# Performance work log

Hardware: AMD Instinct MI355X
Metric: run time of the kernel (lower is better)

## Reference

```python
import jax, jax.numpy as jnp
import numpy as np

B, H, W, C = 64, 56, 56, 256
ROUTES = 4
CONV_OUT = 64


def setup_inputs() -> dict:
    key = jax.random.key(0)
    k1, k2, k3 = jax.random.split(key, 3)
    inputs = jax.random.normal(k1, (B, H, W, C), dtype=jnp.float32)
    # he_normal init for conv kernel (HWIO), zeros bias (keras defaults)
    fan_in = 3 * 3 * C
    conv_w = jax.random.normal(k2, (3, 3, C, CONV_OUT), dtype=jnp.float32) * np.sqrt(2.0 / fan_in)
    conv_b = jnp.zeros((CONV_OUT,), dtype=jnp.float32)
    # glorot_uniform for dense (keras default)
    limit = np.sqrt(6.0 / (CONV_OUT + ROUTES))
    fc_w = jax.random.uniform(k3, (CONV_OUT, ROUTES), dtype=jnp.float32, minval=-limit, maxval=limit)
    fc_b = jnp.zeros((ROUTES,), dtype=jnp.float32)
    return {"inputs": inputs, "conv_w": conv_w, "conv_b": conv_b, "fc_w": fc_w, "fc_b": fc_b}


def reference(inputs, conv_w, conv_b, fc_w, fc_b):
    routes = fc_b.shape[0]
    # route predictor: conv 3x3 stride 2 valid -> global avg pool -> dense logits
    y = jax.lax.conv_general_dilated(
        inputs, conv_w, window_strides=(2, 2), padding="VALID",
        dimension_numbers=("NHWC", "HWIO", "NHWC"))
    y = y + conv_b  # (B, H', W', 64)
    pooled = jnp.mean(y, axis=(1, 2))  # (B, 64)
    logits = pooled @ fc_w + fc_b      # (B, routes)
    route_width = inputs.shape[-1] // routes
    route = jnp.argmax(logits, axis=-1)  # (B,)
    # per-example channel-group gather: channels [r*w, (r+1)*w)
    idx = route[:, None] * route_width + jnp.arange(route_width)  # (B, w)
    x = jnp.take_along_axis(inputs, idx[:, None, None, :], axis=-1)  # (B, H, W, w)
    return (x, logits)
```

## Files before the change

### kernel.cpp

```cpp
#include <hip/hip_runtime.h>
#include <cstdint>
#include <cstddef>

#define Bn 64
#define Hn 56
#define Wn 56
#define Cn 256
#define RWn 64
#define XSZ ((size_t)Bn * Hn * Wn * RWn)
#define RSTRIDE (Wn * Cn)

__device__ __forceinline__ void f4add(float4& a, const float4& v) {
    a.x += v.x; a.y += v.y; a.z += v.z; a.w += v.w;
}
__device__ __forceinline__ float4 f4sub(const float4& a, const float4& b) {
    return make_float4(a.x - b.x, a.y - b.y, a.z - b.z, a.w - b.w);
}

__global__ __launch_bounds__(256, 4) void kA_col(
        const float* __restrict__ in, float* __restrict__ V) {
    const int blk  = blockIdx.x;
    const int b    = blk / (Wn / 4);
    const int wg   = blk - b * (Wn / 4);
    const int lane = threadIdx.x & 63;
    const int wave = threadIdx.x >> 6;
    const int w    = wg * 4 + wave;

    const float* col = in + ((size_t)b * Hn * Wn + (size_t)w) * Cn + (size_t)lane * 4;

    float4 A = make_float4(0.f, 0.f, 0.f, 0.f);
    float4 B = make_float4(0.f, 0.f, 0.f, 0.f);
#pragma unroll
    for (int h = 0; h < Hn; h += 2) {
        f4add(A, *(const float4*)(col + (size_t)h * RSTRIDE));
        f4add(B, *(const float4*)(col + (size_t)(h + 1) * RSTRIDE));
    }
    const float4 r0  = *(const float4*)(col);
    const float4 r54 = *(const float4*)(col + (size_t)54 * RSTRIDE);
    const float4 r55 = *(const float4*)(col + (size_t)55 * RSTRIDE);

    const float4 T0 = f4sub(A, r54);
    const float4 T2 = f4sub(A, r0);
    const float4 T1 = f4sub(B, r55);

    float4* op = (float4*)(V + (((size_t)b * Wn + w) * 3) * 256) + lane;
    op[0]       = T0;
    op[64]      = T1;
    op[128]     = T2;
}

__global__ __launch_bounds__(256) void kB_logits(
        const float* __restrict__ V,
        const float* __restrict__ convw, const float* __restrict__ convb,
        const float* __restrict__ fcw,   const float* __restrict__ fcb,
        float* __restrict__ out_logits, int* __restrict__ routes) {
    const int b = blockIdx.x;
    const int t = threadIdx.x;
    __shared__ float sS[9 * 256];
    __shared__ float pP[4][64];
    __shared__ float pld[64];
    __shared__ float lgt[4];

    const float* Vb = V + (size_t)b * Wn * 3 * 256;
    float Ae[3] = {0.f, 0.f, 0.f};
    float Bo[3] = {0.f, 0.f, 0.f};
#pragma unroll
    for (int w = 0; w < Wn; w += 2) {
#pragma unroll
        for (int kh = 0; kh < 3; ++kh) {
            Ae[kh] += Vb[((w    ) * 3 + kh) * 256 + t];
            Bo[kh] += Vb[((w + 1) * 3 + kh) * 256 + t];
        }
    }
#pragma unroll
    for (int kh = 0; kh < 3; ++kh) {
        const float t0  = Vb[(0  * 3 + kh) * 256 + t];
        const float t54 = Vb[(54 * 3 + kh) * 256 + t];
        const float t55 = Vb[(55 * 3 + kh) * 256 + t];
        sS[(kh * 3 + 0) * 256 + t] = Ae[kh] - t54;
        sS[(kh * 3 + 1) * 256 + t] = Bo[kh] - t55;
        sS[(kh * 3 + 2) * 256 + t] = Ae[kh] - t0;
    }
    __syncthreads();

    {
        const int co = t & 63, part = t >> 6;
        float a = 0.f;
#pragma unroll
        for (int k = 0; k < 9; ++k) {
            const int cb = part * 64;
#pragma unroll 8
            for (int ci = 0; ci < 64; ++ci)
                a += sS[k * 256 + cb + ci] * convw[(size_t)(k * 256 + cb + ci) * 64 + co];
        }
        pP[part][co] = a;
    }
    __syncthreads();

    if (t < 64)
        pld[t] = (pP[0][t] + pP[1][t] + pP[2][t] + pP[3][t]) * (1.f / 729.f) + convb[t];
    __syncthreads();

    if (t < 4) {
        float a = fcb[t];
#pragma unroll
        for (int co = 0; co < 64; ++co) a += pld[co] * fcw[co * 4 + t];
        lgt[t] = a;
        out_logits[b * 4 + t] = a;
    }
    __syncthreads();

    if (t == 0) {
        int bi = 0; float best = lgt[0];
#pragma unroll
        for (int r = 1; r < 4; ++r) if (lgt[r] > best) { best = lgt[r]; bi = r; }
        routes[b] = bi;
    }
}

__global__ __launch_bounds__(256) void kC_gather(
        const float* __restrict__ in, const int* __restrict__ routes,
        float* __restrict__ out) {
    const size_t idx = (size_t)blockIdx.x * 256 + threadIdx.x;
    const size_t pix = idx >> 4;
    const int   f4i  = (int)(idx & 15);
    const int   b    = (int)(pix / (Hn * Wn));
    const int   r    = routes[b];
    const float4 v = *(const float4*)(in + pix * (size_t)Cn
                                      + (size_t)r * RWn + (size_t)f4i * 4);
    ((float4*)out)[idx] = v;
}

extern "C" void kernel_launch(void* const* d_in, const int* in_sizes, int n_in,
                              void* d_out, int out_size, void* d_ws, size_t ws_size,
                              hipStream_t stream) {
    const float* in    = (const float*)d_in[0];
    const float* convw = (const float*)d_in[1];
    const float* convb = (const float*)d_in[2];
    const float* fcw   = (const float*)d_in[3];
    const float* fcb   = (const float*)d_in[4];
    float* out = (float*)d_out;

    const size_t vBytes = (size_t)Bn * Wn * 3 * 256 * sizeof(float);
    float* V      = (float*)d_ws;
    int*   routes = (int*)((char*)d_ws + vBytes);

    kA_col   <<<Bn * (Wn / 4), 256, 0, stream>>>(in, V);
    kB_logits<<<Bn,            256, 0, stream>>>(V, convw, convb, fcw, fcb,
                                                 out + XSZ, routes);
    kC_gather<<<12544,         256, 0, stream>>>(in, routes, out);
}
```

Measured before the change: 349.9 us.

## Fuse column-sum and logits kernels via last-block-per-batch atomic counter

Merges the column-reduction kernel and the per-batch logits kernel into one launch. Each block writes its column partial sums, then increments a per-batch atomic counter, and the last block of each batch does the conv-weight reduction, dense layer and argmax. It also reuses the r0/r1/r54/r55 loads inside the accumulation so those rows are not read twice. This removes one kernel launch and its tail but adds a memset launch, threadfences and an atomic, and it serialises each batch's logits work onto a single late block.

```diff
diff --git a/kernel.cpp b/kernel.cpp
--- a/kernel.cpp
+++ b/kernel.cpp
@@ -9,6 +9,7 @@
 #define RWn 64
 #define XSZ ((size_t)Bn * Hn * Wn * RWn)
 #define RSTRIDE (Wn * Cn)
+#define BPB (Wn / 4)
 
 __device__ __forceinline__ void f4add(float4& a, const float4& v) {
     a.x += v.x; a.y += v.y; a.z += v.z; a.w += v.w;
@@ -17,104 +18,122 @@
     return make_float4(a.x - b.x, a.y - b.y, a.z - b.z, a.w - b.w);
 }
 
-__global__ __launch_bounds__(256, 4) void kA_col(
-        const float* __restrict__ in, float* __restrict__ V) {
-    const int blk  = blockIdx.x;
-    const int b    = blk / (Wn / 4);
-    const int wg   = blk - b * (Wn / 4);
-    const int lane = threadIdx.x & 63;
-    const int wave = threadIdx.x >> 6;
-    const int w    = wg * 4 + wave;
-
-    const float* col = in + ((size_t)b * Hn * Wn + (size_t)w) * Cn + (size_t)lane * 4;
-
-    float4 A = make_float4(0.f, 0.f, 0.f, 0.f);
-    float4 B = make_float4(0.f, 0.f, 0.f, 0.f);
-#pragma unroll
-    for (int h = 0; h < Hn; h += 2) {
-        f4add(A, *(const float4*)(col + (size_t)h * RSTRIDE));
-        f4add(B, *(const float4*)(col + (size_t)(h + 1) * RSTRIDE));
-    }
-    const float4 r0  = *(const float4*)(col);
-    const float4 r54 = *(const float4*)(col + (size_t)54 * RSTRIDE);
-    const float4 r55 = *(const float4*)(col + (size_t)55 * RSTRIDE);
-
-    const float4 T0 = f4sub(A, r54);
-    const float4 T2 = f4sub(A, r0);
-    const float4 T1 = f4sub(B, r55);
-
-    float4* op = (float4*)(V + (((size_t)b * Wn + w) * 3) * 256) + lane;
-    op[0]       = T0;
-    op[64]      = T1;
-    op[128]     = T2;
-}
-
-__global__ __launch_bounds__(256) void kB_logits(
-        const float* __restrict__ V,
+__global__ __launch_bounds__(256, 4) void kAB(
+        const float* __restrict__ in,
         const float* __restrict__ convw, const float* __restrict__ convb,
         const float* __restrict__ fcw,   const float* __restrict__ fcb,
+        float* __restrict__ V, int* __restrict__ cnt,
         float* __restrict__ out_logits, int* __restrict__ routes) {
-    const int b = blockIdx.x;
-    const int t = threadIdx.x;
+    const int blk = blockIdx.x;
+    const int t   = threadIdx.x;
+    const int b   = blk / BPB;
+    const int wg  = blk - b * BPB;
+
     __shared__ float sS[9 * 256];
     __shared__ float pP[4][64];
     __shared__ float pld[64];
     __shared__ float lgt[4];
+    __shared__ int   isLast;
 
-    const float* Vb = V + (size_t)b * Wn * 3 * 256;
-    float Ae[3] = {0.f, 0.f, 0.f};
-    float Bo[3] = {0.f, 0.f, 0.f};
+    {
+        const int lane = t & 63;
+        const int wave = t >> 6;
+        const int w    = wg * 4 + wave;
+
+        const float* col = in + ((size_t)b * Hn * Wn + (size_t)w) * Cn
+                              + (size_t)lane * 4;
+
+        const float4 r0 = *(const float4*)(col);
+        const float4 r1 = *(const float4*)(col + (size_t)RSTRIDE);
+        float4 A  = r0;
+        float4 Bv = r1;
 #pragma unroll
-    for (int w = 0; w < Wn; w += 2) {
+        for (int h = 2; h < 54; h += 2) {
+            f4add(A,  *(const float4*)(col + (size_t)h * RSTRIDE));
+            f4add(Bv, *(const float4*)(col + (size_t)(h + 1) * RSTRIDE));
+        }
+        const float4 r54 = *(const float4*)(col + (size_t)54 * RSTRIDE);
+        const float4 r55 = *(const float4*)(col + (size_t)55 * RSTRIDE);
+        f4add(A, r54);
+        f4add(Bv, r55);
+
+        const float4 T0 = f4sub(A,  r54);
+        const float4 T2 = f4sub(A,  r0);
+        const float4 T1 = f4sub(Bv, r55);
+
+        float4* op = (float4*)(V + (((size_t)b * Wn + w) * 3) * 256) + lane;
+        op[0]   = T0;
+        op[64]  = T1;
+        op[128] = T2;
+    }
+
+    __threadfence();
+    __syncthreads();
+    if (t == 0)
+        isLast = (atomicAdd(&cnt[b], 1) == BPB - 1);
+    __syncthreads();
+    if (!isLast) return;
+    __threadfence();
+
+    {
+        const float* Vb = V + (size_t)b * Wn * 3 * 256;
+        float Ae[3] = {0.f, 0.f, 0.f};
+        float Bo[3] = {0.f, 0.f, 0.f};
+#pragma unroll
+        for (int w = 0; w < Wn; w += 2) {
+#pragma unroll
+            for (int kh = 0; kh < 3; ++kh) {
+                Ae[kh] += Vb[((w    ) * 3 + kh) * 256 + t];
+                Bo[kh] += Vb[((w + 1) * 3 + kh) * 256 + t];
+            }
+        }
 #pragma unroll
         for (int kh = 0; kh < 3; ++kh) {
-            Ae[kh] += Vb[((w    ) * 3 + kh) * 256 + t];
-            Bo[kh] += Vb[((w + 1) * 3 + kh) * 256 + t];
+            const float t0  = Vb[(0  * 3 + kh) * 256 + t];
+            const float t54 = Vb[(54 * 3 + kh) * 256 + t];
+            const float t55 = Vb[(55 * 3 + kh) * 256 + t];
+            sS[(kh * 3 + 0) * 256 + t] = Ae[kh] - t54;
+            sS[(kh * 3 + 1) * 256 + t] = Bo[kh] - t55;
+            sS[(kh * 3 + 2) * 256 + t] = Ae[kh] - t0;
         }
-    }
+        __syncthreads();
+
+        {
+            const int co = t & 63, part = t >> 6;
+            float a = 0.f;
 #pragma unroll
-    for (int kh = 0; kh < 3; ++kh) {
-        const float t0  = Vb[(0  * 3 + kh) * 256 + t];
-        const float t54 = Vb[(54 * 3 + kh) * 256 + t];
-        const float t55 = Vb[(55 * 3 + kh) * 256 + t];
-        sS[(kh * 3 + 0) * 256 + t] = Ae[kh] - t54;
-        sS[(kh * 3 + 1) * 256 + t] = Bo[kh] - t55;
-        sS[(kh * 3 + 2) * 256 + t] = Ae[kh] - t0;
-    }
-    __syncthreads();
+            for (int k = 0; k < 9; ++k) {
+                const int cb = part * 64;
+#pragma unroll 8
+                for (int ci = 0; ci < 64; ++ci)
+                    a += sS[k * 256 + cb + ci]
+                       * convw[(size_t)(k * 256 + cb + ci) * 64 + co];
+            }
+            pP[part][co] = a;
+        }
+        __syncthreads();
 
-    {
-        const int co = t & 63, part = t >> 6;
-        float a = 0.f;
+        if (t < 64)
+            pld[t] = (pP[0][t] + pP[1][t] + pP[2][t] + pP[3][t])
+                     * (1.f / 729.f) + convb[t];
+        __syncthreads();
+
+        if (t < 4) {
+            float a = fcb[t];
 #pragma unroll
-        for (int k = 0; k < 9; ++k) {
-            const int cb = part * 64;
-#pragma unroll 8
-            for (int ci = 0; ci < 64; ++ci)
-                a += sS[k * 256 + cb + ci] * convw[(size_t)(k * 256 + cb + ci) * 64 + co];
+            for (int co = 0; co < 64; ++co) a += pld[co] * fcw[co * 4 + t];
+            lgt[t] = a;
+            out_logits[b * 4 + t] = a;
         }
-        pP[part][co] = a;
-    }
-    __syncthreads();
+        __syncthreads();
 
-    if (t < 64)
-        pld[t] = (pP[0][t] + pP[1][t] + pP[2][t] + pP[3][t]) * (1.f / 729.f) + convb[t];
-    __syncthreads();
-
-    if (t < 4) {
-        float a = fcb[t];
+        if (t == 0) {
+            int bi = 0; float best = lgt[0];
 #pragma unroll
-        for (int co = 0; co < 64; ++co) a += pld[co] * fcw[co * 4 + t];
-        lgt[t] = a;
-        out_logits[b * 4 + t] = a;
-    }
-    __syncthreads();
-
-    if (t == 0) {
-        int bi = 0; float best = lgt[0];
-#pragma unroll
-        for (int r = 1; r < 4; ++r) if (lgt[r] > best) { best = lgt[r]; bi = r; }
-        routes[b] = bi;
+            for (int r = 1; r < 4; ++r)
+                if (lgt[r] > best) { best = lgt[r]; bi = r; }
+            routes[b] = bi;
+        }
     }
 }
 
@@ -144,9 +163,10 @@
     const size_t vBytes = (size_t)Bn * Wn * 3 * 256 * sizeof(float);
     float* V      = (float*)d_ws;
     int*   routes = (int*)((char*)d_ws + vBytes);
+    int*   cnt    = routes + Bn;
 
-    kA_col   <<<Bn * (Wn / 4), 256, 0, stream>>>(in, V);
-    kB_logits<<<Bn,            256, 0, stream>>>(V, convw, convb, fcw, fcb,
-                                                 out + XSZ, routes);
-    kC_gather<<<12544,         256, 0, stream>>>(in, routes, out);
+    hipMemsetAsync(cnt, 0, Bn * sizeof(int), stream);
+    kAB<<<Bn * BPB, 256, 0, stream>>>(in, convw, convb, fcw, fcb,
+                                      V, cnt, out + XSZ, routes);
+    kC_gather<<<12544, 256, 0, stream>>>(in, routes, out);
 }
```

After: 539.8 us. 1.54x slower.
